# Performance work log

Hardware: AMD Instinct MI355X
Metric: run time of the kernel (lower is better)

## Reference

```python
import jax, jax.numpy as jnp
import numpy as np

N_CONS, N_VARS, N_EDGES, N_CAND = 100000, 200000, 8000000, 20000
C_FEAT, V_FEAT = 5, 19


def setup_inputs() -> dict:
    key = jax.random.key(0)
    k1, k2, k3, k4, k5, k6 = jax.random.split(key, 6)
    constraint = jax.random.normal(k1, (N_CONS, C_FEAT), dtype=jnp.float32)
    variable = jax.random.normal(k2, (N_VARS, V_FEAT), dtype=jnp.float32)
    c_edge_index = jax.random.randint(k3, (N_EDGES,), 0, N_CONS, dtype=jnp.int64)
    v_edge_index = jax.random.randint(k4, (N_EDGES,), 0, N_VARS, dtype=jnp.int64)
    cv_edge_index = jnp.stack([c_edge_index, v_edge_index], axis=0)  # [2, E]
    edge_attr = jax.random.normal(k5, (N_EDGES,), dtype=jnp.float32)
    cand_mask = jax.random.randint(k6, (N_CAND,), 0, N_VARS, dtype=jnp.int64)
    return {
        "constraint": constraint,
        "variable": variable,
        "cv_edge_index": cv_edge_index,
        "edge_attr": edge_attr,
        "cand_mask": cand_mask,
    }


def reference(constraint, variable, cv_edge_index, edge_attr, cand_mask):
    # Expression encoded in from_expression:
    #   variable_1_5   = variable[:, 5][v_edge_index]       (gather var feat to edges)
    #   constraint_1_2 = constraint[:, 2][c_edge_index]     (gather cons feat to edges)
    #   msg   = variable_1_5 * edge_attr + constraint_1_2   (edge elementwise)
    #   agg   = scatter_sum(msg, v_edge_index, n_vars)      (scatter to variables)
    #   res   = agg * variable[:, 0] + sqrt(abs(variable[:, 3]))
    #   return res[cand_mask]
    c_edge_index = cv_edge_index[0]
    v_edge_index = cv_edge_index[1]
    variable_1_5 = variable[:, 5][v_edge_index]      # [E]
    constraint_1_2 = constraint[:, 2][c_edge_index]  # [E]
    msg = variable_1_5 * edge_attr + constraint_1_2  # [E]
    agg = jax.ops.segment_sum(msg, v_edge_index, num_segments=variable.shape[0])  # [n_vars]
    result = agg * variable[:, 0] + jnp.sqrt(jnp.abs(variable[:, 3]))
    return result[cand_mask]
```

## Files before the change

kernel.cpp:

```cpp
#include <hip/hip_runtime.h>
#include <math.h>

#define N_CONS  100000
#define N_VARS  200000
#define N_EDGES 8000000
#define N_CAND  20000
#define C_FEAT  5
#define V_FEAT  19
#define BM_WORDS_PAD  6400
#define ACC_SLOTS     20000
#define EDGE_BLOCKS   256
#define CID_BLOCKS    ((ACC_SLOTS + 255) / 256)

__global__ void pack_kernel(const float* __restrict__ variable,
                            const float* __restrict__ constraint,
                            const int* __restrict__ cand,
                            float* __restrict__ var5,
                            float* __restrict__ cons2,
                            unsigned int* __restrict__ bitmap) {
    int i = blockIdx.x * blockDim.x + threadIdx.x;
    if (i < N_VARS) var5[i]  = variable[i * V_FEAT + 5];
    if (i < N_CONS) cons2[i] = constraint[i * C_FEAT + 2];
    if (i < N_CAND) {
        int v = cand[i];
        atomicOr(&bitmap[v >> 5], 1u << (v & 31));
    }
}

__global__ void __launch_bounds__(1024)
scan_kernel(const unsigned int* __restrict__ bitmap,
            uint2* __restrict__ bp) {
    __shared__ unsigned int wsum[16];
    const int CH = 7;
    int t = threadIdx.x;
    int lane = t & 63, wid = t >> 6;
    int base = t * CH;
    unsigned int w_loc[CH];
    unsigned int pf_loc[CH];
    unsigned int sum = 0;
#pragma unroll
    for (int j = 0; j < CH; ++j) {
        int w = base + j;
        unsigned int word = (w < BM_WORDS_PAD) ? bitmap[w] : 0u;
        w_loc[j]  = word;
        pf_loc[j] = sum;
        sum += __popc(word);
    }
    unsigned int inc = sum;
#pragma unroll
    for (int off = 1; off < 64; off <<= 1) {
        unsigned int n = __shfl_up(inc, off, 64);
        if (lane >= off) inc += n;
    }
    if (lane == 63) wsum[wid] = inc;
    __syncthreads();
    if (wid == 0 && lane < 16) {
        unsigned int v = wsum[lane];
#pragma unroll
        for (int off = 1; off < 16; off <<= 1) {
            unsigned int n = __shfl_up(v, off, 16);
            if (lane >= off) v += n;
        }
        wsum[lane] = v;
    }
    __syncthreads();
    unsigned int ebase = inc - sum + (wid ? wsum[wid - 1] : 0u);
#pragma unroll
    for (int j = 0; j < CH; ++j) {
        int w = base + j;
        if (w < BM_WORDS_PAD) bp[w] = make_uint2(w_loc[j], ebase + pf_loc[j]);
    }
}

__global__ void __launch_bounds__(1024, 4)
edge_kernel(const int* __restrict__ c_idx,
            const int* __restrict__ v_idx,
            const float* __restrict__ edge_attr,
            const float* __restrict__ var5,
            const float* __restrict__ cons2,
            const uint2* __restrict__ bp,
            float* __restrict__ partials) {
    __shared__ uint2 lds_bp[BM_WORDS_PAD];
    __shared__ float lds_acc[ACC_SLOTS];

    {
        const uint4* src = (const uint4*)bp;
        uint4* dst = (uint4*)lds_bp;
        for (int j = threadIdx.x; j < BM_WORDS_PAD / 2; j += blockDim.x)
            dst[j] = src[j];
        for (int j = threadIdx.x; j < ACC_SLOTS; j += blockDim.x)
            lds_acc[j] = 0.0f;
    }
    __syncthreads();

    const int nch = N_EDGES / 8;
    const int stride = gridDim.x * blockDim.x;
    const int4*   v4 = (const int4*)v_idx;
    const int4*   c4 = (const int4*)c_idx;
    const float4* e4 = (const float4*)edge_attr;

    for (int g = blockIdx.x * blockDim.x + threadIdx.x; g < nch; g += stride) {
        int4   va = v4[2 * g],  vb = v4[2 * g + 1];
        int4   ca = c4[2 * g],  cb = c4[2 * g + 1];
        float4 ea = e4[2 * g],  eb = e4[2 * g + 1];

        int   vv[8] = { va.x, va.y, va.z, va.w, vb.x, vb.y, vb.z, vb.w };
        int   cc[8] = { ca.x, ca.y, ca.z, ca.w, cb.x, cb.y, cb.z, cb.w };
        float ee[8] = { ea.x, ea.y, ea.z, ea.w, eb.x, eb.y, eb.z, eb.w };

        bool keep[8];
        int  cid[8];
#pragma unroll
        for (int k = 0; k < 8; ++k) {
            uint2 e2 = lds_bp[vv[k] >> 5];
            keep[k] = (e2.x >> (vv[k] & 31)) & 1u;
            cid[k]  = (int)e2.y + __popc(e2.x & ((1u << (vv[k] & 31)) - 1u));
        }

        float v5[8], c2[8];
#pragma unroll
        for (int k = 0; k < 8; ++k) {
            v5[k] = var5[keep[k] ? vv[k] : 0];
            c2[k] = cons2[keep[k] ? cc[k] : 0];
        }
        __builtin_amdgcn_sched_barrier(0);

#pragma unroll
        for (int k = 0; k < 8; ++k) {
            if (keep[k])
                atomicAdd(&lds_acc[cid[k]], v5[k] * ee[k] + c2[k]);
        }
    }
    __syncthreads();

    {
        float4* dst = (float4*)(partials + (size_t)blockIdx.x * ACC_SLOTS);
        const float4* src = (const float4*)lds_acc;
        for (int j = threadIdx.x; j < ACC_SLOTS / 4; j += blockDim.x)
            dst[j] = src[j];
    }
}

__global__ void reduce_kernel(const float* __restrict__ partials,
                              float* __restrict__ agg2) {
    int cid = blockIdx.x * 256 + threadIdx.x;
    if (cid >= ACC_SLOTS) return;
    float s = 0.0f;
#pragma unroll 8
    for (int k = 0; k < EDGE_BLOCKS; ++k)
        s += partials[(size_t)k * ACC_SLOTS + cid];
    agg2[cid] = s;
}

__global__ void out_kernel(const int* __restrict__ cand,
                           const float* __restrict__ agg2,
                           const uint2* __restrict__ bp,
                           const float* __restrict__ variable,
                           float* __restrict__ out) {
    int i = blockIdx.x * blockDim.x + threadIdx.x;
    if (i >= N_CAND) return;
    int v = cand[i];
    uint2 e2 = bp[v >> 5];
    int cid = (int)e2.y + __popc(e2.x & ((1u << (v & 31)) - 1u));
    out[i] = agg2[cid] * variable[v * V_FEAT + 0] + sqrtf(fabsf(variable[v * V_FEAT + 3]));
}

extern "C" void kernel_launch(void* const* d_in, const int* in_sizes, int n_in,
                              void* d_out, int out_size, void* d_ws, size_t ws_size,
                              hipStream_t stream) {
    const float* constraint = (const float*)d_in[0];
    const float* variable   = (const float*)d_in[1];
    const int*   cv_edge    = (const int*)d_in[2];
    const float* edge_attr  = (const float*)d_in[3];
    const int*   cand_mask  = (const int*)d_in[4];
    float* out = (float*)d_out;

    const int* c_idx = cv_edge;
    const int* v_idx = cv_edge + N_EDGES;

    float* var5  = (float*)d_ws;
    float* cons2 = var5 + N_VARS;
    unsigned int* bitmap = (unsigned int*)(cons2 + N_CONS);
    uint2* bp            = (uint2*)(bitmap + BM_WORDS_PAD);
    float* partials      = (float*)(bp + BM_WORDS_PAD);
    float* agg2          = partials + (size_t)EDGE_BLOCKS * ACC_SLOTS;

    hipMemsetAsync(bitmap, 0, BM_WORDS_PAD * sizeof(unsigned int), stream);

    {
        int threads = 256;
        int blocks = (N_VARS + threads - 1) / threads;
        pack_kernel<<<blocks, threads, 0, stream>>>(variable, constraint, cand_mask,
                                                    var5, cons2, bitmap);
    }
    scan_kernel<<<1, 1024, 0, stream>>>(bitmap, bp);
    edge_kernel<<<EDGE_BLOCKS, 1024, 0, stream>>>(c_idx, v_idx, edge_attr,
                                                  var5, cons2, bp, partials);
    reduce_kernel<<<CID_BLOCKS, 256, 0, stream>>>(partials, agg2);
    {
        int threads = 256;
        int blocks = (N_CAND + threads - 1) / threads;
        out_kernel<<<blocks, threads, 0, stream>>>(cand_mask, agg2, bp, variable, out);
    }
}
```

Measured before the change: 61.18 us.

## Fuse bitmap prefix scan into edge kernel, add nontemporal loads and branchy gathers

```diff
diff --git a/kernel.cpp b/kernel.cpp
--- a/kernel.cpp
+++ b/kernel.cpp
@@ -11,6 +11,9 @@
 #define ACC_SLOTS     20000
 #define EDGE_BLOCKS   256
 #define CID_BLOCKS    ((ACC_SLOTS + 255) / 256)
+
+typedef int   i4 __attribute__((ext_vector_type(4)));
+typedef float f4 __attribute__((ext_vector_type(4)));
 
 __global__ void pack_kernel(const float* __restrict__ variable,
                             const float* __restrict__ constraint,
@@ -27,117 +30,112 @@
     }
 }
 
-__global__ void __launch_bounds__(1024)
-scan_kernel(const unsigned int* __restrict__ bitmap,
-            uint2* __restrict__ bp) {
-    __shared__ unsigned int wsum[16];
-    const int CH = 7;
-    int t = threadIdx.x;
-    int lane = t & 63, wid = t >> 6;
-    int base = t * CH;
-    unsigned int w_loc[CH];
-    unsigned int pf_loc[CH];
-    unsigned int sum = 0;
-#pragma unroll
-    for (int j = 0; j < CH; ++j) {
-        int w = base + j;
-        unsigned int word = (w < BM_WORDS_PAD) ? bitmap[w] : 0u;
-        w_loc[j]  = word;
-        pf_loc[j] = sum;
-        sum += __popc(word);
-    }
-    unsigned int inc = sum;
-#pragma unroll
-    for (int off = 1; off < 64; off <<= 1) {
-        unsigned int n = __shfl_up(inc, off, 64);
-        if (lane >= off) inc += n;
-    }
-    if (lane == 63) wsum[wid] = inc;
-    __syncthreads();
-    if (wid == 0 && lane < 16) {
-        unsigned int v = wsum[lane];
-#pragma unroll
-        for (int off = 1; off < 16; off <<= 1) {
-            unsigned int n = __shfl_up(v, off, 16);
-            if (lane >= off) v += n;
-        }
-        wsum[lane] = v;
-    }
-    __syncthreads();
-    unsigned int ebase = inc - sum + (wid ? wsum[wid - 1] : 0u);
-#pragma unroll
-    for (int j = 0; j < CH; ++j) {
-        int w = base + j;
-        if (w < BM_WORDS_PAD) bp[w] = make_uint2(w_loc[j], ebase + pf_loc[j]);
-    }
-}
-
 __global__ void __launch_bounds__(1024, 4)
 edge_kernel(const int* __restrict__ c_idx,
             const int* __restrict__ v_idx,
             const float* __restrict__ edge_attr,
             const float* __restrict__ var5,
             const float* __restrict__ cons2,
-            const uint2* __restrict__ bp,
+            const unsigned int* __restrict__ bitmap,
+            uint2* __restrict__ bpg,
             float* __restrict__ partials) {
     __shared__ uint2 lds_bp[BM_WORDS_PAD];
     __shared__ float lds_acc[ACC_SLOTS];
-
-    {
-        const uint4* src = (const uint4*)bp;
-        uint4* dst = (uint4*)lds_bp;
-        for (int j = threadIdx.x; j < BM_WORDS_PAD / 2; j += blockDim.x)
+    __shared__ unsigned int wsum[16];
+
+    unsigned int* stage = (unsigned int*)lds_acc;
+    {
+        const uint4* src = (const uint4*)bitmap;
+        uint4* dst = (uint4*)stage;
+        for (int j = threadIdx.x; j < BM_WORDS_PAD / 4; j += blockDim.x)
             dst[j] = src[j];
-        for (int j = threadIdx.x; j < ACC_SLOTS; j += blockDim.x)
-            lds_acc[j] = 0.0f;
-    }
+    }
+    __syncthreads();
+
+    {
+        const int CH = 7;
+        int t = threadIdx.x, lane = t & 63, wid = t >> 6;
+        int base = t * CH;
+        unsigned int w_loc[CH], pf_loc[CH], sum = 0;
+#pragma unroll
+        for (int j = 0; j < CH; ++j) {
+            int w = base + j;
+            unsigned int word = (w < BM_WORDS_PAD) ? stage[w] : 0u;
+            w_loc[j]  = word;
+            pf_loc[j] = sum;
+            sum += __popc(word);
+        }
+        unsigned int inc = sum;
+#pragma unroll
+        for (int off = 1; off < 64; off <<= 1) {
+            unsigned int n = __shfl_up(inc, off, 64);
+            if (lane >= off) inc += n;
+        }
+        if (lane == 63) wsum[wid] = inc;
+        __syncthreads();
+        if (wid == 0 && lane < 16) {
+            unsigned int v = wsum[lane];
+#pragma unroll
+            for (int off = 1; off < 16; off <<= 1) {
+                unsigned int n = __shfl_up(v, off, 16);
+                if (lane >= off) v += n;
+            }
+            wsum[lane] = v;
+        }
+        __syncthreads();
+        unsigned int ebase = inc - sum + (wid ? wsum[wid - 1] : 0u);
+#pragma unroll
+        for (int j = 0; j < CH; ++j) {
+            int w = base + j;
+            if (w < BM_WORDS_PAD) lds_bp[w] = make_uint2(w_loc[j], ebase + pf_loc[j]);
+        }
+    }
+    __syncthreads();
+    for (int j = threadIdx.x; j < ACC_SLOTS; j += blockDim.x)
+        lds_acc[j] = 0.0f;
     __syncthreads();
 
     const int nch = N_EDGES / 8;
     const int stride = gridDim.x * blockDim.x;
-    const int4*   v4 = (const int4*)v_idx;
-    const int4*   c4 = (const int4*)c_idx;
-    const float4* e4 = (const float4*)edge_attr;
+    const i4* v4 = (const i4*)v_idx;
+    const i4* c4 = (const i4*)c_idx;
+    const f4* e4 = (const f4*)edge_attr;
 
     for (int g = blockIdx.x * blockDim.x + threadIdx.x; g < nch; g += stride) {
-        int4   va = v4[2 * g],  vb = v4[2 * g + 1];
-        int4   ca = c4[2 * g],  cb = c4[2 * g + 1];
-        float4 ea = e4[2 * g],  eb = e4[2 * g + 1];
-
-        int   vv[8] = { va.x, va.y, va.z, va.w, vb.x, vb.y, vb.z, vb.w };
-        int   cc[8] = { ca.x, ca.y, ca.z, ca.w, cb.x, cb.y, cb.z, cb.w };
-        float ee[8] = { ea.x, ea.y, ea.z, ea.w, eb.x, eb.y, eb.z, eb.w };
-
-        bool keep[8];
-        int  cid[8];
-#pragma unroll
-        for (int k = 0; k < 8; ++k) {
-            uint2 e2 = lds_bp[vv[k] >> 5];
-            keep[k] = (e2.x >> (vv[k] & 31)) & 1u;
-            cid[k]  = (int)e2.y + __popc(e2.x & ((1u << (vv[k] & 31)) - 1u));
-        }
-
-        float v5[8], c2[8];
-#pragma unroll
-        for (int k = 0; k < 8; ++k) {
-            v5[k] = var5[keep[k] ? vv[k] : 0];
-            c2[k] = cons2[keep[k] ? cc[k] : 0];
-        }
-        __builtin_amdgcn_sched_barrier(0);
-
-#pragma unroll
-        for (int k = 0; k < 8; ++k) {
-            if (keep[k])
-                atomicAdd(&lds_acc[cid[k]], v5[k] * ee[k] + c2[k]);
-        }
-    }
-    __syncthreads();
-
-    {
-        float4* dst = (float4*)(partials + (size_t)blockIdx.x * ACC_SLOTS);
-        const float4* src = (const float4*)lds_acc;
+        i4 va = __builtin_nontemporal_load(v4 + 2 * g);
+        i4 vb = __builtin_nontemporal_load(v4 + 2 * g + 1);
+        i4 ca = __builtin_nontemporal_load(c4 + 2 * g);
+        i4 cb = __builtin_nontemporal_load(c4 + 2 * g + 1);
+        f4 ea = __builtin_nontemporal_load(e4 + 2 * g);
+        f4 eb = __builtin_nontemporal_load(e4 + 2 * g + 1);
+
+#define PROC(vv, cc, ee)                                                     \
+        {                                                                    \
+            uint2 e2 = lds_bp[(vv) >> 5];                                    \
+            if ((e2.x >> ((vv) & 31)) & 1u) {                                \
+                int cid = (int)e2.y +                                        \
+                          __popc(e2.x & ((1u << ((vv) & 31)) - 1u));         \
+                atomicAdd(&lds_acc[cid],                                     \
+                          var5[vv] * (ee) + cons2[cc]);                      \
+            }                                                                \
+        }
+        PROC(va[0], ca[0], ea[0])  PROC(va[1], ca[1], ea[1])
+        PROC(va[2], ca[2], ea[2])  PROC(va[3], ca[3], ea[3])
+        PROC(vb[0], cb[0], eb[0])  PROC(vb[1], cb[1], eb[1])
+        PROC(vb[2], cb[2], eb[2])  PROC(vb[3], cb[3], eb[3])
+#undef PROC
+    }
+    __syncthreads();
+
+    {
+        f4* dst = (f4*)(partials + (size_t)blockIdx.x * ACC_SLOTS);
+        const f4* src = (const f4*)lds_acc;
         for (int j = threadIdx.x; j < ACC_SLOTS / 4; j += blockDim.x)
-            dst[j] = src[j];
+            __builtin_nontemporal_store(src[j], dst + j);
+    }
+    if (blockIdx.x == 0) {
+        for (int j = threadIdx.x; j < BM_WORDS_PAD; j += blockDim.x)
+            bpg[j] = lds_bp[j];
     }
 }
 
@@ -148,19 +146,19 @@
     float s = 0.0f;
 #pragma unroll 8
     for (int k = 0; k < EDGE_BLOCKS; ++k)
-        s += partials[(size_t)k * ACC_SLOTS + cid];
+        s += __builtin_nontemporal_load(&partials[(size_t)k * ACC_SLOTS + cid]);
     agg2[cid] = s;
 }
 
 __global__ void out_kernel(const int* __restrict__ cand,
                            const float* __restrict__ agg2,
-                           const uint2* __restrict__ bp,
+                           const uint2* __restrict__ bpg,
                            const float* __restrict__ variable,
                            float* __restrict__ out) {
     int i = blockIdx.x * blockDim.x + threadIdx.x;
     if (i >= N_CAND) return;
     int v = cand[i];
-    uint2 e2 = bp[v >> 5];
+    uint2 e2 = bpg[v >> 5];
     int cid = (int)e2.y + __popc(e2.x & ((1u << (v & 31)) - 1u));
     out[i] = agg2[cid] * variable[v * V_FEAT + 0] + sqrtf(fabsf(variable[v * V_FEAT + 3]));
 }
@@ -181,8 +179,8 @@
     float* var5  = (float*)d_ws;
     float* cons2 = var5 + N_VARS;
     unsigned int* bitmap = (unsigned int*)(cons2 + N_CONS);
-    uint2* bp            = (uint2*)(bitmap + BM_WORDS_PAD);
-    float* partials      = (float*)(bp + BM_WORDS_PAD);
+    uint2* bpg           = (uint2*)(bitmap + BM_WORDS_PAD);
+    float* partials      = (float*)(bpg + BM_WORDS_PAD);
     float* agg2          = partials + (size_t)EDGE_BLOCKS * ACC_SLOTS;
 
     hipMemsetAsync(bitmap, 0, BM_WORDS_PAD * sizeof(unsigned int), stream);
@@ -193,13 +191,13 @@
         pack_kernel<<<blocks, threads, 0, stream>>>(variable, constraint, cand_mask,
                                                     var5, cons2, bitmap);
     }
-    scan_kernel<<<1, 1024, 0, stream>>>(bitmap, bp);
     edge_kernel<<<EDGE_BLOCKS, 1024, 0, stream>>>(c_idx, v_idx, edge_attr,
-                                                  var5, cons2, bp, partials);
+                                                  var5, cons2, bitmap, bpg,
+                                                  partials);
     reduce_kernel<<<CID_BLOCKS, 256, 0, stream>>>(partials, agg2);
     {
         int threads = 256;
         int blocks = (N_CAND + threads - 1) / threads;
-        out_kernel<<<blocks, threads, 0, stream>>>(cand_mask, agg2, bp, variable, out);
-    }
-}
+        out_kernel<<<blocks, threads, 0, stream>>>(cand_mask, agg2, bpg, variable, out);
+    }
+}
```

Result: slower. 72.89 us (+19.1%).
